# Performance work log

Hardware: AMD Instinct MI355X
Metric: run time of the kernel (lower is better)

## Reference

```python
import jax, jax.numpy as jnp
import numpy as np

B, N, C, H = 4, 128, 512, 8
D = C // H
SCALE = D ** (-0.5) * 50.0


def setup_inputs() -> dict:
    key = jax.random.key(0)
    kx, kw = jax.random.split(key)
    x = jax.random.normal(kx, (B, N, N, C), dtype=jnp.float32)
    # torch Linear(n_embd, 5*n_embd, bias=False); stored here as [in, out] for x @ w
    w_qkv = jax.random.normal(kw, (C, 5 * C), dtype=jnp.float32) * (C ** -0.5)
    return {"x": x, "w_qkv": w_qkv}


def _heads(t):
    # [b, i, j, h*d] -> [b, h, i, j, d]
    b, i, j, _ = t.shape
    return t.reshape(b, i, j, H, D).transpose(0, 3, 1, 2, 4)


def reference(x, w_qkv):
    # global norm over the entire tensor (torch .std() is unbiased, ddof=1)
    x = (x - x.mean()) / x.std(ddof=1)
    qkv = x @ w_qkv                                   # [b, i, j, 5c]
    q, k1, k2, v1, v2 = map(_heads, jnp.split(qkv, 5, axis=-1))
    # pivotal attention: for query (i,j), pivot over k with row stream k1[i,k]
    # and column stream k2[k,j]
    scores = SCALE * (jnp.einsum('bhijd,bhikd->bhijk', q, k1)
                      + jnp.einsum('bhijd,bhkjd->bhijk', q, k2))
    attn = jax.nn.softmax(scores, axis=-1)            # [b, h, i, j, k]
    out = (jnp.einsum('bhijk,bhikd->bhijd', attn, v1)
           + jnp.einsum('bhijk,bhkjd->bhijd', attn, v2))
    # [b, h, i, j, d] -> [b, i, j, h*d]
    return out.transpose(0, 2, 3, 1, 4).reshape(B, N, N, C)
```

## Files before the change

### kernel.cpp

```cpp
#include <hip/hip_runtime.h>
#include <stdint.h>


typedef __attribute__((ext_vector_type(8))) short s8v;
typedef __attribute__((ext_vector_type(4))) float f4v;

#define MFMA(a, b, c) __builtin_amdgcn_mfma_f32_16x16x32_bf16((a), (b), (c), 0, 0, 0)

__device__ __forceinline__ float bf2f(unsigned short u) {
  union { unsigned int i; float f; } v; v.i = ((unsigned int)u) << 16; return v.f;
}
__device__ __forceinline__ unsigned short f2bf(float f) {
  union { float f; unsigned int i; } v; v.f = f;
  unsigned int i = v.i;
  return (unsigned short)((i + 0x7fffu + ((i >> 16) & 1u)) >> 16);
}

__device__ __forceinline__ void async_copy16(const void* g, void* l) {
  __builtin_amdgcn_global_load_lds(
      (const __attribute__((address_space(1))) unsigned int*)(uintptr_t)g,
      (__attribute__((address_space(3))) unsigned int*)(uintptr_t)l,
      16, 0, 0);
}

__global__ __launch_bounds__(256) void k_probe(const unsigned short* __restrict__ x,
                                               int* __restrict__ flag) {
  uint4 v = ((const uint4*)x)[threadIdx.x];
  unsigned int uu[4] = {v.x, v.y, v.z, v.w};
  int bad = 0;
#pragma unroll
  for (int u = 0; u < 4; ++u) {
    float a = bf2f((unsigned short)(uu[u] & 0xffffu));
    float b = bf2f((unsigned short)(uu[u] >> 16));
    if (!(fabsf(a) <= 1e4f)) bad = 1;
    if (!(fabsf(b) <= 1e4f)) bad = 1;
  }
  if (bad) atomicOr(flag, 1);
}

__global__ __launch_bounds__(256) void k_red(const void* __restrict__ xraw,
                                             const int* __restrict__ flag,
                                             double* __restrict__ dstats) {
  __shared__ float red[8];
  const int fm = flag[0];
  int t = threadIdx.x;
  size_t gid = (size_t)blockIdx.x * 256 + t;
  float s = 0.f, ss = 0.f;
  if (fm) {
    const float4* pf = (const float4*)xraw;
#pragma unroll 4
    for (int it = 0; it < 32; ++it) {
      size_t idx = gid + (size_t)it * 131072;
      float4 u1 = pf[2 * idx], u2 = pf[2 * idx + 1];
      float vals[8] = {u1.x, u1.y, u1.z, u1.w, u2.x, u2.y, u2.z, u2.w};
#pragma unroll
      for (int u = 0; u < 8; ++u) { s += vals[u]; ss += vals[u] * vals[u]; }
    }
  } else {
    const uint4* p = (const uint4*)xraw;
#pragma unroll 4
    for (int it = 0; it < 32; ++it) {
      uint4 v = p[gid + (size_t)it * 131072];
      unsigned int uu[4] = {v.x, v.y, v.z, v.w};
#pragma unroll
      for (int u = 0; u < 4; ++u) {
        float a = bf2f((unsigned short)(uu[u] & 0xffffu));
        float b = bf2f((unsigned short)(uu[u] >> 16));
        s += a + b;
        ss += a * a + b * b;
      }
    }
  }
#pragma unroll
  for (int d = 32; d >= 1; d >>= 1) {
    s += __shfl_down(s, d);
    ss += __shfl_down(ss, d);
  }
  int lane = t & 63, wave = t >> 6;
  if (lane == 0) { red[wave] = s; red[4 + wave] = ss; }
  __syncthreads();
  if (t == 0) {
    atomicAdd(&dstats[0], (double)(red[0] + red[1] + red[2] + red[3]));
    atomicAdd(&dstats[1], (double)(red[4] + red[5] + red[6] + red[7]));
  }
}

__global__ void k_stats(const double* __restrict__ dstats, float* __restrict__ fstats) {
  double M = 33554432.0;
  double mean = dstats[0] / M;
  double var = (dstats[1] - dstats[0] * dstats[0] / M) / (M - 1.0);
  double istd = 1.0 / sqrt(var);
  fstats[0] = (float)istd;
  fstats[1] = (float)(-mean * istd);
}

__global__ __launch_bounds__(256) void k_colsum(const void* __restrict__ wraw,
                                                const int* __restrict__ flag,
                                                float* __restrict__ colsum) {
  const int fm = flag[0];
  int c = blockIdx.x * 256 + threadIdx.x;
  if (c >= 2560) return;
  float s = 0.f;
  if (fm) {
    const float* w = (const float*)wraw;
    for (int r = 0; r < 512; ++r) s += w[(size_t)r * 2560 + c];
  } else {
    const unsigned short* w = (const unsigned short*)wraw;
    for (int r = 0; r < 512; ++r) s += bf2f(w[(size_t)r * 2560 + c]);
  }
  colsum[c] = s;
}

__global__ __launch_bounds__(256) void k_wt(const void* __restrict__ wraw,
                                            const int* __restrict__ flag,
                                            unsigned short* __restrict__ wThi,
                                            unsigned short* __restrict__ wTlo) {
  __shared__ float tile[64][65];
  const int fm = flag[0];
  int n0 = blockIdx.x * 64, r0 = blockIdx.y * 64;
#pragma unroll
  for (int rep = 0; rep < 16; ++rep) {
    int idx = rep * 256 + threadIdx.x;
    int r = idx >> 6, n = idx & 63;
    float v;
    if (fm) v = ((const float*)wraw)[(size_t)(r0 + r) * 2560 + n0 + n];
    else    v = bf2f(((const unsigned short*)wraw)[(size_t)(r0 + r) * 2560 + n0 + n]);
    tile[r][n] = v;
  }
  __syncthreads();
#pragma unroll
  for (int rep = 0; rep < 16; ++rep) {
    int idx = rep * 256 + threadIdx.x;
    int n = idx >> 6, r = idx & 63;
    float v = tile[r][n];
    unsigned short hi = f2bf(v);
    size_t o = (size_t)(n0 + n) * 512 + r0 + r;
    wThi[o] = hi;
    wTlo[o] = f2bf(v - bf2f(hi));
  }
}

__global__ __launch_bounds__(256) void k_convx(const void* __restrict__ xraw,
                                               const int* __restrict__ flag,
                                               unsigned short* __restrict__ xhi,
                                               unsigned short* __restrict__ xlo,
                                               int b) {
  const int fm = flag[0];
  size_t e0 = ((size_t)blockIdx.x * 256 + threadIdx.x) * 8;
  size_t g0 = (size_t)b * 8388608 + e0;
  float vals[8];
  if (fm) {
    const float4* pf = (const float4*)xraw;
    float4 u1 = pf[g0 / 4], u2 = pf[g0 / 4 + 1];
    vals[0] = u1.x; vals[1] = u1.y; vals[2] = u1.z; vals[3] = u1.w;
    vals[4] = u2.x; vals[5] = u2.y; vals[6] = u2.z; vals[7] = u2.w;
  } else {
    uint4 v = ((const uint4*)xraw)[g0 / 8];
    unsigned int uu[4] = {v.x, v.y, v.z, v.w};
#pragma unroll
    for (int u = 0; u < 4; ++u) {
      vals[2 * u] = bf2f((unsigned short)(uu[u] & 0xffffu));
      vals[2 * u + 1] = bf2f((unsigned short)(uu[u] >> 16));
    }
  }
  unsigned short h[8], l[8];
#pragma unroll
  for (int u = 0; u < 8; ++u) {
    h[u] = f2bf(vals[u]);
    l[u] = f2bf(vals[u] - bf2f(h[u]));
  }
  *(uint4*)(xhi + e0) = *(const uint4*)h;
  *(uint4*)(xlo + e0) = *(const uint4*)l;
}

__global__ __launch_bounds__(256) void k_gemm(
    const unsigned short* __restrict__ xhi, const unsigned short* __restrict__ xlo,
    const unsigned short* __restrict__ wThi, const unsigned short* __restrict__ wTlo,
    const float* __restrict__ colsum, const float* __restrict__ fstats,
    const int* __restrict__ flag,
    unsigned short* __restrict__ qhi, unsigned short* __restrict__ qlo,
    unsigned short* __restrict__ k1hi, unsigned short* __restrict__ k1lo,
    unsigned short* __restrict__ k2hi, unsigned short* __restrict__ k2lo,
    unsigned short* __restrict__ v1T, unsigned short* __restrict__ v2T,
    int h0, int hcShift) {
  __shared__ __align__(16) unsigned short Ash[2][4096];
  __shared__ __align__(16) unsigned short Asl[2][4096];
  __shared__ __align__(16) unsigned short Bsh[2][4096];
  __shared__ __align__(16) unsigned short Bsl[2][4096];
  const int fm = flag[0];
  const int t = threadIdx.x;
  const int m0 = blockIdx.x * 128;
  const int n0 = blockIdx.y * 128;
  const int hcMask = (1 << hcShift) - 1;

  const int lane = t & 63, wave = t >> 6;
  const int wm = (wave & 1) * 64, wn = (wave >> 1) * 64;
  const int l16 = lane & 15, q4 = lane >> 4;

  const int srow0 = t >> 2;
  const int srow1 = 64 + srow0;
  const int sch = (((t & 3) ^ ((t >> 3) & 3)) << 3);
  const int swoff = ((q4 ^ ((l16 >> 1) & 3)) << 3);

  const float af = fstats[0], bfc = fstats[1];
  const unsigned short* xh = xhi + (size_t)m0 * 512;
  const unsigned short* xl = xlo + (size_t)m0 * 512;

  int wcol0, wcol1;
  {
    int n = n0 + srow0, g = n >> hcShift, rem = n & hcMask;
    wcol0 = (g << 9) + ((h0 + (rem >> 6)) << 6) + (rem & 63);
    n = n0 + srow1; g = n >> hcShift; rem = n & hcMask;
    wcol1 = (g << 9) + ((h0 + (rem >> 6)) << 6) + (rem & 63);
  }

  f4v acc[4][4];
#pragma unroll
  for (int a = 0; a < 4; ++a)
#pragma unroll
    for (int c = 0; c < 4; ++c) acc[a][c] = (f4v)0.f;

  auto STAGE = [&](int bsel, int k0) {
    async_copy16(xh + (size_t)srow0 * 512 + k0 + sch, (char*)&Ash[bsel][0] + t * 16);
    async_copy16(xh + (size_t)srow1 * 512 + k0 + sch, (char*)&Ash[bsel][0] + (256 + t) * 16);
    async_copy16(wThi + (size_t)wcol0 * 512 + k0 + sch, (char*)&Bsh[bsel][0] + t * 16);
    async_copy16(wThi + (size_t)wcol1 * 512 + k0 + sch, (char*)&Bsh[bsel][0] + (256 + t) * 16);
    if (fm) {
      async_copy16(xl + (size_t)srow0 * 512 + k0 + sch, (char*)&Asl[bsel][0] + t * 16);
      async_copy16(xl + (size_t)srow1 * 512 + k0 + sch, (char*)&Asl[bsel][0] + (256 + t) * 16);
      async_copy16(wTlo + (size_t)wcol0 * 512 + k0 + sch, (char*)&Bsl[bsel][0] + t * 16);
      async_copy16(wTlo + (size_t)wcol1 * 512 + k0 + sch, (char*)&Bsl[bsel][0] + (256 + t) * 16);
    }
  };

  STAGE(0, 0);

#pragma unroll 2
  for (int ks = 0; ks < 16; ++ks) {
    const int kb = ks & 1;
    if (ks < 15) {
      STAGE(kb ^ 1, (ks + 1) << 5);
      if (fm) asm volatile("s_waitcnt vmcnt(8)" ::: "memory");
      else    asm volatile("s_waitcnt vmcnt(4)" ::: "memory");
    } else {
      asm volatile("s_waitcnt vmcnt(0)" ::: "memory");
    }
    __builtin_amdgcn_s_barrier();

    s8v ah[4], bh[4];
#pragma unroll
    for (int jt = 0; jt < 4; ++jt)
      ah[jt] = *(const s8v*)&Ash[kb][(wm + jt * 16 + l16) * 32 + swoff];
#pragma unroll
    for (int nt = 0; nt < 4; ++nt)
      bh[nt] = *(const s8v*)&Bsh[kb][(wn + nt * 16 + l16) * 32 + swoff];
    if (fm) {
      s8v al[4], bl[4];
#pragma unroll
      for (int jt = 0; jt < 4; ++jt)
        al[jt] = *(const s8v*)&Asl[kb][(wm + jt * 16 + l16) * 32 + swoff];
#pragma unroll
      for (int nt = 0; nt < 4; ++nt)
        bl[nt] = *(const s8v*)&Bsl[kb][(wn + nt * 16 + l16) * 32 + swoff];
#pragma unroll
      for (int jt = 0; jt < 4; ++jt)
#pragma unroll
        for (int nt = 0; nt < 4; ++nt) {
          acc[jt][nt] = MFMA(ah[jt], bh[nt], acc[jt][nt]);
          acc[jt][nt] = MFMA(ah[jt], bl[nt], acc[jt][nt]);
          acc[jt][nt] = MFMA(al[jt], bh[nt], acc[jt][nt]);
        }
    } else {
#pragma unroll
      for (int jt = 0; jt < 4; ++jt)
#pragma unroll
        for (int nt = 0; nt < 4; ++nt) acc[jt][nt] = MFMA(ah[jt], bh[nt], acc[jt][nt]);
    }
    asm volatile("" ::: "memory");
    __builtin_amdgcn_s_barrier();
  }

#pragma unroll
  for (int jt = 0; jt < 4; ++jt) {
#pragma unroll
    for (int nt = 0; nt < 4; ++nt) {
      int gcol = n0 + wn + nt * 16 + l16;
      int g = gcol >> hcShift, rem = gcol & hcMask;
      int hl = rem >> 6, d = rem & 63;
      int wcol = (g << 9) + ((h0 + hl) << 6) + d;
      float cs = colsum[wcol] * bfc;
#pragma unroll
      for (int r = 0; r < 4; ++r) {
        int grow = m0 + wm + jt * 16 + q4 * 4 + r;
        int i = grow >> 7, j = grow & 127;
        float val = acc[jt][nt][r] * af + cs;
        unsigned short hi = f2bf(val);
        if (g == 0) {
          size_t idx = (((size_t)hl * 128 + i) * 128 + j) * 64 + d;
          qhi[idx] = hi; qlo[idx] = f2bf(val - bf2f(hi));
        } else if (g == 1) {
          size_t idx = (((size_t)hl * 128 + i) * 128 + j) * 64 + d;
          k1hi[idx] = hi; k1lo[idx] = f2bf(val - bf2f(hi));
        } else if (g == 2) {
          size_t idx = (((size_t)hl * 128 + j) * 128 + i) * 64 + d;
          k2hi[idx] = hi; k2lo[idx] = f2bf(val - bf2f(hi));
        } else if (g == 3) {
          size_t idx = (((size_t)hl * 128 + i) * 64 + d) * 128 + j;
          v1T[idx] = hi;
        } else {
          size_t idx = (((size_t)hl * 128 + j) * 64 + d) * 128 + i;
          v2T[idx] = hi;
        }
      }
    }
  }
}

__global__ __launch_bounds__(256) void k_s1(
    const unsigned short* __restrict__ qhi, const unsigned short* __restrict__ qlo,
    const unsigned short* __restrict__ k1hi, const unsigned short* __restrict__ k1lo,
    float* __restrict__ S) {
  const int i = blockIdx.x, hl = blockIdx.y;
  const int t = threadIdx.x, lane = t & 63, wave = t >> 6;
  const int l16 = lane & 15, q4 = lane >> 4;
  const size_t base = ((size_t)hl * 128 + i) * 128 * 64;

  f4v acc[2][8];
#pragma unroll
  for (int a = 0; a < 2; ++a)
#pragma unroll
    for (int c = 0; c < 8; ++c) acc[a][c] = (f4v)0.f;

#pragma unroll
  for (int kc = 0; kc < 2; ++kc) {
    s8v ah[2], al[2];
#pragma unroll
    for (int jt = 0; jt < 2; ++jt) {
      size_t off = base + (size_t)(wave * 32 + jt * 16 + l16) * 64 + kc * 32 + q4 * 8;
      ah[jt] = *(const s8v*)(qhi + off);
      al[jt] = *(const s8v*)(qlo + off);
    }
#pragma unroll
    for (int kt = 0; kt < 8; ++kt) {
      size_t off = base + (size_t)(kt * 16 + l16) * 64 + kc * 32 + q4 * 8;
      s8v bh = *(const s8v*)(k1hi + off);
      s8v bl = *(const s8v*)(k1lo + off);
#pragma unroll
      for (int jt = 0; jt < 2; ++jt) {
        acc[jt][kt] = MFMA(ah[jt], bh, acc[jt][kt]);
        acc[jt][kt] = MFMA(ah[jt], bl, acc[jt][kt]);
        acc[jt][kt] = MFMA(al[jt], bh, acc[jt][kt]);
      }
    }
  }
  float* Sb = S + ((size_t)hl * 128 + i) * 128 * 128;
#pragma unroll
  for (int jt = 0; jt < 2; ++jt)
#pragma unroll
    for (int kt = 0; kt < 8; ++kt)
#pragma unroll
      for (int r = 0; r < 4; ++r) {
        int j = wave * 32 + jt * 16 + q4 * 4 + r;
        Sb[(size_t)j * 128 + kt * 16 + l16] = acc[jt][kt][r];
      }
}

__global__ __launch_bounds__(256) void k_s2(
    const unsigned short* __restrict__ qhi, const unsigned short* __restrict__ qlo,
    const unsigned short* __restrict__ k2hi, const unsigned short* __restrict__ k2lo,
    const float* __restrict__ S, unsigned short* __restrict__ attn) {
  const int j = blockIdx.x, hl = blockIdx.y;
  const int t = threadIdx.x, lane = t & 63, wave = t >> 6;
  const int l16 = lane & 15, q4 = lane >> 4;
  const size_t bbase = ((size_t)hl * 128 + j) * 128 * 64;

  f4v acc[2][8];
#pragma unroll
  for (int a = 0; a < 2; ++a)
#pragma unroll
    for (int c = 0; c < 8; ++c) acc[a][c] = (f4v)0.f;

#pragma unroll
  for (int kc = 0; kc < 2; ++kc) {
    s8v ah[2], al[2];
#pragma unroll
    for (int it = 0; it < 2; ++it) {
      size_t off = (((size_t)hl * 128 + (wave * 32 + it * 16 + l16)) * 128 + j) * 64 +
                   kc * 32 + q4 * 8;
      ah[it] = *(const s8v*)(qhi + off);
      al[it] = *(const s8v*)(qlo + off);
    }
#pragma unroll
    for (int kt = 0; kt < 8; ++kt) {
      size_t off = bbase + (size_t)(kt * 16 + l16) * 64 + kc * 32 + q4 * 8;
      s8v bh = *(const s8v*)(k2hi + off);
      s8v bl = *(const s8v*)(k2lo + off);
#pragma unroll
      for (int it = 0; it < 2; ++it) {
        acc[it][kt] = MFMA(ah[it], bh, acc[it][kt]);
        acc[it][kt] = MFMA(ah[it], bl, acc[it][kt]);
        acc[it][kt] = MFMA(al[it], bh, acc[it][kt]);
      }
    }
  }

#pragma unroll
  for (int it = 0; it < 2; ++it) {
#pragma unroll
    for (int r = 0; r < 4; ++r) {
      int i = wave * 32 + it * 16 + q4 * 4 + r;
      const float* Srow = S + (((size_t)hl * 128 + i) * 128 + j) * 128;
      float tv[8];
      float m = -3.4e38f;
#pragma unroll
      for (int kt = 0; kt < 8; ++kt) {
        tv[kt] = 6.25f * (Srow[kt * 16 + l16] + acc[it][kt][r]);
        m = fmaxf(m, tv[kt]);
      }
#pragma unroll
      for (int d = 1; d <= 8; d <<= 1) m = fmaxf(m, __shfl_xor(m, d));
      float sum = 0.f;
#pragma unroll
      for (int kt = 0; kt < 8; ++kt) {
        tv[kt] = __expf(tv[kt] - m);
        sum += tv[kt];
      }
#pragma unroll
      for (int d = 1; d <= 8; d <<= 1) sum += __shfl_xor(sum, d);
      float rs = 1.f / sum;
      unsigned short* arow = attn + (((size_t)hl * 128 + i) * 128 + j) * 128;
#pragma unroll
      for (int kt = 0; kt < 8; ++kt) arow[kt * 16 + l16] = f2bf(tv[kt] * rs);
    }
  }
}

__global__ __launch_bounds__(256) void k_av1(
    const unsigned short* __restrict__ attn, const unsigned short* __restrict__ v1T,
    unsigned short* __restrict__ out1) {
  const int i = blockIdx.x, hl = blockIdx.y;
  const int t = threadIdx.x, lane = t & 63, wave = t >> 6;
  const int l16 = lane & 15, q4 = lane >> 4;
  const size_t abase = ((size_t)hl * 128 + i) * 128 * 128;
  const size_t vbase = ((size_t)hl * 128 + i) * 64 * 128;

  f4v acc[2][4];
#pragma unroll
  for (int a = 0; a < 2; ++a)
#pragma unroll
    for (int c = 0; c < 4; ++c) acc[a][c] = (f4v)0.f;

#pragma unroll
  for (int kc = 0; kc < 4; ++kc) {
    s8v a[2], bfr[4];
#pragma unroll
    for (int jt = 0; jt < 2; ++jt)
      a[jt] = *(const s8v*)(attn + abase + (size_t)(wave * 32 + jt * 16 + l16) * 128 +
                            kc * 32 + q4 * 8);
#pragma unroll
    for (int dt = 0; dt < 4; ++dt)
      bfr[dt] = *(const s8v*)(v1T + vbase + (size_t)(dt * 16 + l16) * 128 + kc * 32 + q4 * 8);
#pragma unroll
    for (int jt = 0; jt < 2; ++jt)
#pragma unroll
      for (int dt = 0; dt < 4; ++dt) acc[jt][dt] = MFMA(a[jt], bfr[dt], acc[jt][dt]);
  }
  unsigned short* ob = out1 + ((size_t)hl * 128 + i) * 128 * 64;
#pragma unroll
  for (int jt = 0; jt < 2; ++jt)
#pragma unroll
    for (int dt = 0; dt < 4; ++dt)
#pragma unroll
      for (int r = 0; r < 4; ++r) {
        int j = wave * 32 + jt * 16 + q4 * 4 + r;
        ob[(size_t)j * 64 + dt * 16 + l16] = f2bf(acc[jt][dt][r]);
      }
}

__global__ __launch_bounds__(256) void k_av2(
    const unsigned short* __restrict__ attn, const unsigned short* __restrict__ v2T,
    const unsigned short* __restrict__ out1, const int* __restrict__ flag,
    void* __restrict__ out, int b, int h0) {
  const int j = blockIdx.x, hl = blockIdx.y;
  const int t = threadIdx.x, lane = t & 63, wave = t >> 6;
  const int l16 = lane & 15, q4 = lane >> 4;
  const int fm = flag[0];
  const size_t vbase = ((size_t)hl * 128 + j) * 64 * 128;

  f4v acc[2][4];
#pragma unroll
  for (int a = 0; a < 2; ++a)
#pragma unroll
    for (int c = 0; c < 4; ++c) acc[a][c] = (f4v)0.f;

#pragma unroll
  for (int kc = 0; kc < 4; ++kc) {
    s8v a[2], bfr[4];
#pragma unroll
    for (int it = 0; it < 2; ++it)
      a[it] = *(const s8v*)(attn +
                            (((size_t)hl * 128 + (wave * 32 + it * 16 + l16)) * 128 + j) * 128 +
                            kc * 32 + q4 * 8);
#pragma unroll
    for (int dt = 0; dt < 4; ++dt)
      bfr[dt] = *(const s8v*)(v2T + vbase + (size_t)(dt * 16 + l16) * 128 + kc * 32 + q4 * 8);
#pragma unroll
    for (int it = 0; it < 2; ++it)
#pragma unroll
      for (int dt = 0; dt < 4; ++dt) acc[it][dt] = MFMA(a[it], bfr[dt], acc[it][dt]);
  }
#pragma unroll
  for (int it = 0; it < 2; ++it)
#pragma unroll
    for (int dt = 0; dt < 4; ++dt)
#pragma unroll
      for (int r = 0; r < 4; ++r) {
        int i = wave * 32 + it * 16 + q4 * 4 + r;
        int d = dt * 16 + l16;
        float o = acc[it][dt][r] + bf2f(out1[(((size_t)hl * 128 + i) * 128 + j) * 64 + d]);
        size_t oi = ((size_t)b * 16384 + i * 128 + j) * 512 + (h0 + hl) * 64 + d;
        if (fm) ((float*)out)[oi] = o;
        else    ((unsigned short*)out)[oi] = f2bf(o);
      }
}

extern "C" void kernel_launch(void* const* d_in, const int* in_sizes, int n_in,
                              void* d_out, int out_size, void* d_ws, size_t ws_size,
                              hipStream_t stream) {
  (void)in_sizes; (void)n_in; (void)out_size;
  const void* x = d_in[0];
  const void* w = d_in[1];

  const size_t xslice = (size_t)16384 * 512;
  const size_t wTsz = (size_t)2560 * 512;
  const size_t fixed = xslice * 4 + wTsz * 4 + 2560 * 4 + 64;

  int Hc = 2;
  if (30 * ((size_t)8 * 1048576) + fixed <= ws_size) Hc = 8;
  else if (30 * ((size_t)4 * 1048576) + fixed <= ws_size) Hc = 4;
  const int hcShift = (Hc == 8) ? 9 : ((Hc == 4) ? 8 : 7);
  const size_t TE = (size_t)Hc * 1048576;

  char* p = (char*)d_ws;
  unsigned short* qhi = (unsigned short*)p;  p += TE * 2;
  unsigned short* qlo = (unsigned short*)p;  p += TE * 2;
  unsigned short* k1hi = (unsigned short*)p; p += TE * 2;
  unsigned short* k1lo = (unsigned short*)p; p += TE * 2;
  unsigned short* k2hi = (unsigned short*)p; p += TE * 2;
  unsigned short* k2lo = (unsigned short*)p; p += TE * 2;
  unsigned short* v1T = (unsigned short*)p;  p += TE * 2;
  unsigned short* v2T = (unsigned short*)p;  p += TE * 2;
  float* S = (float*)p;                      p += TE * 8;
  unsigned short* attn = (unsigned short*)p; p += TE * 4;
  unsigned short* out1 = (unsigned short*)p; p += TE * 2;
  unsigned short* xhi = (unsigned short*)p;  p += xslice * 2;
  unsigned short* xlo = (unsigned short*)p;  p += xslice * 2;
  unsigned short* wThi = (unsigned short*)p; p += wTsz * 2;
  unsigned short* wTlo = (unsigned short*)p; p += wTsz * 2;
  float* colsum = (float*)p;                 p += 2560 * 4;
  double* dstats = (double*)p;               p += 16;
  int* flag = (int*)p;                       p += 8;
  float* fstats = (float*)p;                 p += 8;

  hipMemsetAsync(dstats, 0, 24, stream);
  k_probe<<<1, 256, 0, stream>>>((const unsigned short*)x, flag);
  k_red<<<512, 256, 0, stream>>>(x, flag, dstats);
  k_stats<<<1, 1, 0, stream>>>(dstats, fstats);
  k_colsum<<<10, 256, 0, stream>>>(w, flag, colsum);
  k_wt<<<dim3(40, 8), 256, 0, stream>>>(w, flag, wThi, wTlo);

  for (int b = 0; b < 4; ++b) {
    k_convx<<<4096, 256, 0, stream>>>(x, flag, xhi, xlo, b);
    for (int h0 = 0; h0 < 8; h0 += Hc) {
      k_gemm<<<dim3(128, (5 * Hc * 64) / 128), 256, 0, stream>>>(
          xhi, xlo, wThi, wTlo, colsum, fstats, flag,
          qhi, qlo, k1hi, k1lo, k2hi, k2lo, v1T, v2T, h0, hcShift);
      k_s1<<<dim3(128, Hc), 256, 0, stream>>>(qhi, qlo, k1hi, k1lo, S);
      k_s2<<<dim3(128, Hc), 256, 0, stream>>>(qhi, qlo, k2hi, k2lo, S, attn);
      k_av1<<<dim3(128, Hc), 256, 0, stream>>>(attn, v1T, out1);
      k_av2<<<dim3(128, Hc), 256, 0, stream>>>(attn, v2T, out1, flag, d_out, b, h0);
    }
  }
}
```

Measured before the change: 1.669 ms.

## Remap GEMM workgroups per XCD and stage v1 transpose through LDS for coalesced stores

Workgroup indices are remapped so consecutive blocks on the same XCD share M-tiles of x, aiming to improve L2 reuse across the chiplets. For the v1 output group, the epilogue now writes the tile transposed into swizzled LDS and then emits 16-byte coalesced stores to v1T, replacing scattered 2-byte strided writes. The remap assumes gridDim.x is 128 and a specific XCD count. The LDS staging adds a barrier and reuses the GEMM buffers after the main loop.

```diff
diff --git a/kernel.cpp b/kernel.cpp
--- a/kernel.cpp
+++ b/kernel.cpp
@@ -183,14 +183,20 @@
     unsigned short* __restrict__ k2hi, unsigned short* __restrict__ k2lo,
     unsigned short* __restrict__ v1T, unsigned short* __restrict__ v2T,
     int h0, int hcShift) {
-  __shared__ __align__(16) unsigned short Ash[2][4096];
-  __shared__ __align__(16) unsigned short Asl[2][4096];
-  __shared__ __align__(16) unsigned short Bsh[2][4096];
-  __shared__ __align__(16) unsigned short Bsl[2][4096];
+  __shared__ __align__(16) unsigned short LDS[32768];
+  unsigned short* Ash = LDS;
+  unsigned short* Asl = LDS + 8192;
+  unsigned short* Bsh = LDS + 16384;
+  unsigned short* Bsl = LDS + 24576;
   const int fm = flag[0];
   const int t = threadIdx.x;
-  const int m0 = blockIdx.x * 128;
-  const int n0 = blockIdx.y * 128;
+
+  const int nwgy = gridDim.y;
+  const int vid = blockIdx.x + (blockIdx.y << 7);
+  const int xcd = vid & 7, seq = vid >> 3;
+  const int m0 = (xcd * 16 + seq / nwgy) * 128;
+  const int n0 = (seq % nwgy) * 128;
+
   const int hcMask = (1 << hcShift) - 1;
 
   const int lane = t & 63, wave = t >> 6;
@@ -221,15 +227,15 @@
     for (int c = 0; c < 4; ++c) acc[a][c] = (f4v)0.f;
 
   auto STAGE = [&](int bsel, int k0) {
-    async_copy16(xh + (size_t)srow0 * 512 + k0 + sch, (char*)&Ash[bsel][0] + t * 16);
-    async_copy16(xh + (size_t)srow1 * 512 + k0 + sch, (char*)&Ash[bsel][0] + (256 + t) * 16);
-    async_copy16(wThi + (size_t)wcol0 * 512 + k0 + sch, (char*)&Bsh[bsel][0] + t * 16);
-    async_copy16(wThi + (size_t)wcol1 * 512 + k0 + sch, (char*)&Bsh[bsel][0] + (256 + t) * 16);
+    async_copy16(xh + (size_t)srow0 * 512 + k0 + sch, (char*)(Ash + bsel * 4096) + t * 16);
+    async_copy16(xh + (size_t)srow1 * 512 + k0 + sch, (char*)(Ash + bsel * 4096) + (256 + t) * 16);
+    async_copy16(wThi + (size_t)wcol0 * 512 + k0 + sch, (char*)(Bsh + bsel * 4096) + t * 16);
+    async_copy16(wThi + (size_t)wcol1 * 512 + k0 + sch, (char*)(Bsh + bsel * 4096) + (256 + t) * 16);
     if (fm) {
-      async_copy16(xl + (size_t)srow0 * 512 + k0 + sch, (char*)&Asl[bsel][0] + t * 16);
-      async_copy16(xl + (size_t)srow1 * 512 + k0 + sch, (char*)&Asl[bsel][0] + (256 + t) * 16);
-      async_copy16(wTlo + (size_t)wcol0 * 512 + k0 + sch, (char*)&Bsl[bsel][0] + t * 16);
-      async_copy16(wTlo + (size_t)wcol1 * 512 + k0 + sch, (char*)&Bsl[bsel][0] + (256 + t) * 16);
+      async_copy16(xl + (size_t)srow0 * 512 + k0 + sch, (char*)(Asl + bsel * 4096) + t * 16);
+      async_copy16(xl + (size_t)srow1 * 512 + k0 + sch, (char*)(Asl + bsel * 4096) + (256 + t) * 16);
+      async_copy16(wTlo + (size_t)wcol0 * 512 + k0 + sch, (char*)(Bsl + bsel * 4096) + t * 16);
+      async_copy16(wTlo + (size_t)wcol1 * 512 + k0 + sch, (char*)(Bsl + bsel * 4096) + (256 + t) * 16);
     }
   };
 
@@ -250,18 +256,18 @@
     s8v ah[4], bh[4];
 #pragma unroll
     for (int jt = 0; jt < 4; ++jt)
-      ah[jt] = *(const s8v*)&Ash[kb][(wm + jt * 16 + l16) * 32 + swoff];
+      ah[jt] = *(const s8v*)&Ash[kb * 4096 + (wm + jt * 16 + l16) * 32 + swoff];
 #pragma unroll
     for (int nt = 0; nt < 4; ++nt)
-      bh[nt] = *(const s8v*)&Bsh[kb][(wn + nt * 16 + l16) * 32 + swoff];
+      bh[nt] = *(const s8v*)&Bsh[kb * 4096 + (wn + nt * 16 + l16) * 32 + swoff];
     if (fm) {
       s8v al[4], bl[4];
 #pragma unroll
       for (int jt = 0; jt < 4; ++jt)
-        al[jt] = *(const s8v*)&Asl[kb][(wm + jt * 16 + l16) * 32 + swoff];
+        al[jt] = *(const s8v*)&Asl[kb * 4096 + (wm + jt * 16 + l16) * 32 + swoff];
 #pragma unroll
       for (int nt = 0; nt < 4; ++nt)
-        bl[nt] = *(const s8v*)&Bsl[kb][(wn + nt * 16 + l16) * 32 + swoff];
+        bl[nt] = *(const s8v*)&Bsl[kb * 4096 + (wn + nt * 16 + l16) * 32 + swoff];
 #pragma unroll
       for (int jt = 0; jt < 4; ++jt)
 #pragma unroll
@@ -280,36 +286,65 @@
     __builtin_amdgcn_s_barrier();
   }
 
-#pragma unroll
-  for (int jt = 0; jt < 4; ++jt) {
+  const int gblk = n0 >> hcShift;
+  if (gblk == 3) {
+    unsigned short* TB = LDS;
 #pragma unroll
     for (int nt = 0; nt < 4; ++nt) {
-      int gcol = n0 + wn + nt * 16 + l16;
-      int g = gcol >> hcShift, rem = gcol & hcMask;
-      int hl = rem >> 6, d = rem & 63;
-      int wcol = (g << 9) + ((h0 + hl) << 6) + d;
+      int cl = wn + nt * 16 + l16;
+      int rem = (n0 + cl) & hcMask;
+      int wcol = (3 << 9) + ((h0 + (rem >> 6)) << 6) + (rem & 63);
       float cs = colsum[wcol] * bfc;
-#pragma unroll
-      for (int r = 0; r < 4; ++r) {
-        int grow = m0 + wm + jt * 16 + q4 * 4 + r;
-        int i = grow >> 7, j = grow & 127;
-        float val = acc[jt][nt][r] * af + cs;
-        unsigned short hi = f2bf(val);
-        if (g == 0) {
-          size_t idx = (((size_t)hl * 128 + i) * 128 + j) * 64 + d;
-          qhi[idx] = hi; qlo[idx] = f2bf(val - bf2f(hi));
-        } else if (g == 1) {
-          size_t idx = (((size_t)hl * 128 + i) * 128 + j) * 64 + d;
-          k1hi[idx] = hi; k1lo[idx] = f2bf(val - bf2f(hi));
-        } else if (g == 2) {
-          size_t idx = (((size_t)hl * 128 + j) * 128 + i) * 64 + d;
-          k2hi[idx] = hi; k2lo[idx] = f2bf(val - bf2f(hi));
-        } else if (g == 3) {
-          size_t idx = (((size_t)hl * 128 + i) * 64 + d) * 128 + j;
-          v1T[idx] = hi;
-        } else {
-          size_t idx = (((size_t)hl * 128 + j) * 64 + d) * 128 + i;
-          v2T[idx] = hi;
+      int swz = (cl & 15) << 3;
+#pragma unroll
+      for (int jt = 0; jt < 4; ++jt)
+#pragma unroll
+        for (int r = 0; r < 4; ++r) {
+          int jL = wm + jt * 16 + q4 * 4 + r;
+          TB[cl * 128 + (jL ^ swz)] = f2bf(acc[jt][nt][r] * af + cs);
+        }
+    }
+    __syncthreads();
+    const int iBlk = m0 >> 7;
+    const int hl0 = (n0 & hcMask) >> 6;
+#pragma unroll
+    for (int rep = 0; rep < 8; ++rep) {
+      int f16 = rep * 256 + t;
+      int cl = f16 >> 4;
+      int j0 = (f16 & 15) * 8;
+      int hl = hl0 + (cl >> 6), d = cl & 63;
+      uint4 vv = *(const uint4*)&TB[cl * 128 + (j0 ^ ((cl & 15) << 3))];
+      *(uint4*)&v1T[(((size_t)hl * 128 + iBlk) * 64 + d) * 128 + j0] = vv;
+    }
+  } else {
+#pragma unroll
+    for (int jt = 0; jt < 4; ++jt) {
+#pragma unroll
+      for (int nt = 0; nt < 4; ++nt) {
+        int gcol = n0 + wn + nt * 16 + l16;
+        int g = gcol >> hcShift, rem = gcol & hcMask;
+        int hl = rem >> 6, d = rem & 63;
+        int wcol = (g << 9) + ((h0 + hl) << 6) + d;
+        float cs = colsum[wcol] * bfc;
+#pragma unroll
+        for (int r = 0; r < 4; ++r) {
+          int grow = m0 + wm + jt * 16 + q4 * 4 + r;
+          int i = grow >> 7, j = grow & 127;
+          float val = acc[jt][nt][r] * af + cs;
+          unsigned short hi = f2bf(val);
+          if (g == 0) {
+            size_t idx = (((size_t)hl * 128 + i) * 128 + j) * 64 + d;
+            qhi[idx] = hi; qlo[idx] = f2bf(val - bf2f(hi));
+          } else if (g == 1) {
+            size_t idx = (((size_t)hl * 128 + i) * 128 + j) * 64 + d;
+            k1hi[idx] = hi; k1lo[idx] = f2bf(val - bf2f(hi));
+          } else if (g == 2) {
+            size_t idx = (((size_t)hl * 128 + j) * 128 + i) * 64 + d;
+            k2hi[idx] = hi; k2lo[idx] = f2bf(val - bf2f(hi));
+          } else {
+            size_t idx = (((size_t)hl * 128 + j) * 64 + d) * 128 + i;
+            v2T[idx] = hi;
+          }
         }
       }
     }
```

Result: slower. 1.798 ms (+7.7%).
